# Kernel optimization log

Measured on AMD Instinct MI355X. Metric: run time of the kernel, lower is better.

The kernel has to match this reference:

```python
import jax, jax.numpy as jnp
import numpy as np

B, N, F_IN = 32, 1024, 64   # batch, num_nodes, diffusion_size[0]
K = 3                        # expansion_step
H = 2                        # num_heads
HID, RAW, OUT, CLS = 128, 128, 128, 2
D1, D2 = 128, 128            # diffusion_size[1], diffusion_size[2]
CAT = D1 + RAW               # concat dim fed to attention (h || h_prime) = 256


def setup_inputs() -> dict:
    key = jax.random.key(0)
    ks = jax.random.split(key, 40)
    g = lambda i, shape: jax.random.normal(ks[i], shape, dtype=jnp.float32) * 0.05
    inp = {
        'X': jax.random.normal(ks[0], (B, N, F_IN), dtype=jnp.float32),
        'A': jax.random.uniform(ks[1], (B, N, N), dtype=jnp.float32),
        # transition tensors / mixing weights (only the 2 layers used in forward)
        'T': g(2, (2, K, N, N)),
        'theta': jnp.full((2, K), 1.0 / K, dtype=jnp.float32),
        # raw feature projection
        'W_raw': g(3, (F_IN, RAW)), 'b_raw': jnp.zeros((RAW,), jnp.float32),
        # diffusion layer linears
        'Wd0': g(4, (F_IN, D1)), 'bd0': jnp.zeros((D1,), jnp.float32),
        'Wd1': g(5, (D1, D2)),   'bd1': jnp.zeros((D2,), jnp.float32),
        # final classifier
        'W_fin': g(6, (OUT, CLS)), 'b_fin': jnp.zeros((CLS,), jnp.float32),
    }
    # two CatMultiAttn blocks: q/k/v projections (CAT->HID), out proj (HID->OUT)
    i = 7
    for l in range(2):
        for nm in ('q', 'k', 'v'):
            inp[f'W{nm}{l}'] = g(i, (CAT, HID)); i += 1
            inp[f'b{nm}{l}'] = jnp.zeros((HID,), jnp.float32)
        inp[f'Wo{l}'] = g(i, (HID, OUT)); i += 1
        inp[f'bo{l}'] = jnp.zeros((OUT,), jnp.float32)
    return inp


def _diffusion(theta_l, T_l, h, A, W, b):
    # Q = sum_k theta_k * T_k  (generalized graph diffusion transition)
    Q = jnp.einsum('k,kij->ij', theta_l, T_l)          # [N,N]
    S = Q[None, :, :] * A                               # [B,N,N] mask by adjacency
    z = jnp.einsum('bij,bjf->bif', S, h)                # diffuse features
    return jax.nn.relu(z @ W + b)


def _cat_attn(h, hp, Wq, bq, Wk, bk, Wv, bv, Wo, bo):
    # concatenate diffused + embedding features, multi-head self-attn over nodes
    x = jnp.concatenate([h, hp], axis=-1)               # [B,N,CAT]
    b, n, _ = x.shape
    q = (x @ Wq + bq).reshape(b, n, H, HID // H)
    k = (x @ Wk + bk).reshape(b, n, H, HID // H)
    v = (x @ Wv + bv).reshape(b, n, H, HID // H)
    scale = jnp.asarray(1.0 / np.sqrt(HID // H), x.dtype)
    s = jnp.einsum('bnhd,bmhd->bhnm', q, k) * scale     # [B,H,N,N]
    p = jax.nn.softmax(s, axis=-1)
    ctx = jnp.einsum('bhnm,bmhd->bnhd', p, v).reshape(b, n, HID)
    return jax.nn.relu(ctx @ Wo + bo)


def reference(X, A, T, theta, W_raw, b_raw, Wd0, bd0, Wd1, bd1,
              W_fin, b_fin,
              Wq0, bq0, Wk0, bk0, Wv0, bv0, Wo0, bo0,
              Wq1, bq1, Wk1, bk1, Wv1, bv1, Wo1, bo1):
    theta_soft = jax.nn.softmax(theta, axis=-1)         # [2,K]
    h_prime = X @ W_raw + b_raw                          # [B,N,RAW]
    # layer 0
    h = _diffusion(theta_soft[0], T[0], X, A, Wd0, bd0)  # [B,N,D1]
    h_prime = _cat_attn(h, h_prime, Wq0, bq0, Wk0, bk0, Wv0, bv0, Wo0, bo0)
    # layer 1 (residual fusion)
    h = _diffusion(theta_soft[1], T[1], h, A, Wd1, bd1)  # [B,N,D2]
    h_prime = h_prime + _cat_attn(h, h_prime, Wq1, bq1, Wk1, bk1, Wv1, bv1, Wo1, bo1)
    return h_prime @ W_fin + b_fin                       # [B,N,CLS]
```

## Files before the change

### kernel.cpp

```cpp
#include <hip/hip_runtime.h>
#include <hip/hip_bf16.h>

typedef __hip_bfloat16 bf16;
typedef __attribute__((ext_vector_type(8))) short s8b;
typedef __attribute__((ext_vector_type(4))) short s4b;
typedef __attribute__((ext_vector_type(4))) float f4;

#define BB   32
#define NN   1024
#define FIN  64
#define HEADS 2
#define DH   64
#define HIDD 128
#define SZQ  ((size_t)BB * NN * HIDD)

__device__ __forceinline__ ushort f2bf(float x) {
    bf16 h = __float2bfloat16(x);
    return *(ushort*)&h;
}
__device__ __forceinline__ float bfbits2f(ushort h) {
    union { uint u; float f; } c; c.u = (uint)h << 16; return c.f;
}
__device__ __forceinline__ uint pk_bf16(float lo, float hi) {
    return (uint)f2bf(lo) | ((uint)f2bf(hi) << 16);
// ... 2 lines not shown
union U4 { short s[4]; s4b v; };
union UQ { ushort u[8]; s8b v; };

__global__ __launch_bounds__(256) void setup_kernel(
        const float* __restrict__ raw, const float* __restrict__ d0,
        const float* __restrict__ d1,
        const float* __restrict__ q0w, const float* __restrict__ k0w,
        const float* __restrict__ v0w, const float* __restrict__ o0w,
        const float* __restrict__ q1w, const float* __restrict__ k1w,
        const float* __restrict__ v1w, const float* __restrict__ o1w,
        ushort* __restrict__ Whi, ushort* __restrict__ Wlo,
        const float* __restrict__ T, const float* __restrict__ theta,
        ushort* __restrict__ Q0hi, ushort* __restrict__ Q0lo,
        ushort* __restrict__ Q1hi, ushort* __restrict__ Q1lo,
        const float* __restrict__ X,
        ushort* __restrict__ XT_hi, ushort* __restrict__ XT_lo) {
    __shared__ float tile[64][65];
    const int bid = blockIdx.x;
    const int t = threadIdx.x;
    if (bid < 1024) {
        int id = bid * 256 + t;
        const float* src; int K, off;
        if      (id <   8192) { src = raw; K =  64; off = 0; }
        else if (id <  16384) { src = d0;  K =  64; off = 8192; }
        else if (id <  32768) { src = d1;  K = 128; off = 16384; }
        else if (id <  65536) { src = q0w; K = 256; off = 32768; }
        else if (id <  98304) { src = k0w; K = 256; off = 65536; }
        else if (id < 131072) { src = v0w; K = 256; off = 98304; }
        else if (id < 147456) { src = o0w; K = 128; off = 131072; }
        else if (id < 180224) { src = q1w; K = 256; off = 147456; }
        else if (id < 212992) { src = k1w; K = 256; off = 180224; }
        else if (id < 245760) { src = v1w; K = 256; off = 212992; }
        else                  { src = o1w; K = 128; off = 245760; }
        int il = id - off;
        int k = il >> 7, c = il & 127;
        float w = src[il];
        ushort h = f2bf(w);
        Whi[off + c * K + k] = h;
        Wlo[off + c * K + k] = f2bf(w - bfbits2f(h));
    } else if (bid < 1536) {
        const int tb = bid - 1024;
        const int b  = tb >> 4;
        const int n0 = (tb & 15) * 64;
        {
            int nl = t >> 2, f0 = (t & 3) * 16;
            const float* xp = X + ((size_t)b * NN + n0 + nl) * 64 + f0;
#pragma unroll
            for (int i = 0; i < 16; i += 4)
                *(float4*)&tile[nl][f0 + i] = *(const float4*)(xp + i);
        }
        __syncthreads();
        {
            int f = t >> 2, n1 = (t & 3) * 16;
            U8 h0, h1, l0, l1;
#pragma unroll
            for (int i = 0; i < 16; i++) {
                float v = tile[n1 + i][f];
                ushort hh = f2bf(v);
                ushort ll = f2bf(v - bfbits2f(hh));
                if (i < 8) { h0.s[i] = (short)hh; l0.s[i] = (short)ll; }
                else       { h1.s[i - 8] = (short)hh; l1.s[i - 8] = (short)ll; }
            }
            size_t gb = ((size_t)b * 64 + f) * NN + n0 + n1;
            *(s8b*)&XT_hi[gb]     = h0.v;  *(s8b*)&XT_hi[gb + 8] = h1.v;
            *(s8b*)&XT_lo[gb]     = l0.v;  *(s8b*)&XT_lo[gb + 8] = l1.v;
        }
    } else {
        const int layer = (bid < 2048) ? 0 : 1;
        ushort* Qhi = layer ? Q1hi : Q0hi;
        ushort* Qlo = layer ? Q1lo : Q0lo;
        float t0 = theta[layer * 3 + 0];
        float t1 = theta[layer * 3 + 1];
        float t2 = theta[layer * 3 + 2];
        float m  = fmaxf(t0, fmaxf(t1, t2));
        float e0 = expf(t0 - m), e1 = expf(t1 - m), e2 = expf(t2 - m);
        float inv = 1.0f / (e0 + e1 + e2);
        e0 *= inv; e1 *= inv; e2 *= inv;
        size_t base = ((size_t)((bid - 1536) & 511) * 256 + t) * 8;
        const float* Tl = T + (size_t)layer * 3 * NN * NN;
        U8 hi, lo;
#pragma unroll
        for (int i = 0; i < 8; i++) {
            float q = e0 * Tl[base + i]
                    + e1 * Tl[base + i + (size_t)NN * NN]
                    + e2 * Tl[base + i + (size_t)2 * NN * NN];
            ushort hh = f2bf(q);
            hi.s[i] = (short)hh;
            lo.s[i] = (short)f2bf(q - bfbits2f(hh));
        }
        *(s8b*)&Qhi[base] = hi.v;
        *(s8b*)&Qlo[base] = lo.v;
    }
}

template<int F, bool WRITE_HT>
__global__ __launch_bounds__(512, 4) void diff_dense_kernel(
        const ushort* __restrict__ Qhi, const ushort* __restrict__ Qlo,
        const float* __restrict__ A,
        const ushort* __restrict__ hT_hi, const ushort* __restrict__ hT_lo,
        const ushort* __restrict__ WT_hi, const ushort* __restrict__ WT_lo,
        const float* __restrict__ bias,
        float* __restrict__ hout,
        ushort* __restrict__ hiT, ushort* __restrict__ loT) {
    constexpr int SS  = 72;
    constexpr int NT  = F / 16;
    constexpr int NCW = NT / 4;
    constexpr int SZ2 = F + 8;
    constexpr int P1 = 2 * 64 * SS + 2 * F * SS;
    constexpr int P2 = 2 * 64 * SZ2 + 2 * 128 * 40;
    __shared__ short smem[(P1 > P2) ? P1 : P2];
    short* Shi = smem;
    short* Slo = Shi + 64 * SS;
    short* Hhi = Slo + 64 * SS;
    short* Hlo = Hhi + (size_t)F * SS;
    short* Zhi = smem;
    short* Zlo = Zhi + 64 * SZ2;
    short* Wsh = Zlo + 64 * SZ2;
    short* Wsl = Wsh + 128 * 40;

    const int bidx = blockIdx.x;
    const int u  = bidx >> 3;
    const int b  = (bidx & 7) + 8 * (u >> 4);
    const int i0 = (u & 15) * 64;
    const int t  = threadIdx.x;
    const int w  = t >> 6, lane = t & 63;
    const int quad = lane >> 4, c = lane & 15;
    const int rh = w >> 2;
    const int ch = w & 3;

    const int srow = t >> 3, scol = (t & 7) * 8;
    const float*  Ap = A   + ((size_t)b * NN + i0 + srow) * NN + scol;
    const ushort* Qh = Qhi + (size_t)(i0 + srow) * NN + scol;
    const ushort* Ql = Qlo + (size_t)(i0 + srow) * NN + scol;
    constexpr int HTR = 512 / F;
    constexpr int HJ  = 64 / HTR;
    constexpr int HV  = HJ / 8;
    const int hrow = t / HTR, hcol = (t % HTR) * HJ;
    const ushort* Hh = hT_hi + ((size_t)b * F + hrow) * NN + hcol;
    const ushort* Hl = hT_lo + ((size_t)b * F + hrow) * NN + hcol;

    f4 acc[2][NCW];
#pragma unroll
    for (int st = 0; st < 2; st++)
#pragma unroll
        for (int i = 0; i < NCW; i++) acc[st][i] = (f4){0.f, 0.f, 0.f, 0.f};

    float4 a0 = *(const float4*)Ap, a1 = *(const float4*)(Ap + 4);
    s8b hhv[HV], hlv[HV];
#pragma unroll
    for (int vv = 0; vv < HV; vv++) {
        hhv[vv] = *(const s8b*)(Hh + 8 * vv);
        hlv[vv] = *(const s8b*)(Hl + 8 * vv);
    }

#pragma unroll 1
    for (int j0 = 0; j0 < NN; j0 += 64) {
        UQ qh, ql;
        qh.v = *(const s8b*)(Qh + j0);
        ql.v = *(const s8b*)(Ql + j0);
        __syncthreads();
        {
            float av[8] = {a0.x, a0.y, a0.z, a0.w, a1.x, a1.y, a1.z, a1.w};
            U8 hi, lo;
#pragma unroll
            for (int i = 0; i < 8; i++) {
                float q = bfbits2f(qh.u[i]) + bfbits2f(ql.u[i]);
                float s = q * av[i];
                ushort hb = f2bf(s);
                hi.s[i] = (short)hb;
                lo.s[i] = (short)f2bf(s - bfbits2f(hb));
            }
            *(s8b*)&Shi[srow * SS + scol] = hi.v;
            *(s8b*)&Slo[srow * SS + scol] = lo.v;
#pragma unroll
            for (int vv = 0; vv < HV; vv++) {
                *(s8b*)&Hhi[hrow * SS + hcol + 8 * vv] = hhv[vv];
                *(s8b*)&Hlo[hrow * SS + hcol + 8 * vv] = hlv[vv];
            }
        }
        if (j0 + 64 < NN) {
            a0 = *(const float4*)(Ap + j0 + 64);
            a1 = *(const float4*)(Ap + j0 + 68);
#pragma unroll
            for (int vv = 0; vv < HV; vv++) {
                hhv[vv] = *(const s8b*)(Hh + j0 + 64 + 8 * vv);
                hlv[vv] = *(const s8b*)(Hl + j0 + 64 + 8 * vv);
            }
        }
        __syncthreads();

#pragma unroll
        for (int ks = 0; ks < 2; ks++) {
            s8b ah0 = *(const s8b*)&Shi[(32 * rh + c) * SS + ks * 32 + quad * 8];
            s8b al0 = *(const s8b*)&Slo[(32 * rh + c) * SS + ks * 32 + quad * 8];
            s8b ah1 = *(const s8b*)&Shi[(32 * rh + 16 + c) * SS + ks * 32 + quad * 8];
            s8b al1 = *(const s8b*)&Slo[(32 * rh + 16 + c) * SS + ks * 32 + quad * 8];
#pragma unroll
            for (int ctn = 0; ctn < NCW; ctn++) {
                const int nt = ch * NCW + ctn;
                s8b bhi = *(const s8b*)&Hhi[(nt * 16 + c) * SS + ks * 32 + quad * 8];
                s8b blo = *(const s8b*)&Hlo[(nt * 16 + c) * SS + ks * 32 + quad * 8];
                acc[0][ctn] = __builtin_amdgcn_mfma_f32_16x16x32_bf16(ah0, bhi, acc[0][ctn], 0, 0, 0);
                acc[0][ctn] = __builtin_amdgcn_mfma_f32_16x16x32_bf16(al0, bhi, acc[0][ctn], 0, 0, 0);
                acc[0][ctn] = __builtin_amdgcn_mfma_f32_16x16x32_bf16(ah0, blo, acc[0][ctn], 0, 0, 0);
                acc[1][ctn] = __builtin_amdgcn_mfma_f32_16x16x32_bf16(ah1, bhi, acc[1][ctn], 0, 0, 0);
                acc[1][ctn] = __builtin_amdgcn_mfma_f32_16x16x32_bf16(al1, bhi, acc[1][ctn], 0, 0, 0);
                acc[1][ctn] = __builtin_amdgcn_mfma_f32_16x16x32_bf16(ah1, blo, acc[1][ctn], 0, 0, 0);
            }
        }
    }

    __syncthreads();
#pragma unroll
    for (int st = 0; st < 2; st++)
#pragma unroll
        for (int ctn = 0; ctn < NCW; ctn++)
#pragma unroll
            for (int r = 0; r < 4; r++) {
                const int row = 32 * rh + 16 * st + quad * 4 + r;
                const int col = (ch * NCW + ctn) * 16 + c;
                float v = acc[st][ctn][r];
                ushort hh = f2bf(v);
                Zhi[row * SZ2 + col] = (short)hh;
                Zlo[row * SZ2 + col] = (short)f2bf(v - bfbits2f(hh));
            }

    const int rh2 = w >> 2;
    const int ch2 = w & 3;
    f4 acc2[2][2];
#pragma unroll
    for (int st = 0; st < 2; st++)
#pragma unroll
        for (int i = 0; i < 2; i++) acc2[st][i] = (f4){0.f, 0.f, 0.f, 0.f};

    constexpr int NKT = F / 32;
    for (int kt = 0; kt < NKT; kt++) {
        __syncthreads();
        {
            int cc = t >> 2, kk = (t & 3) * 8;
            size_t gsrc = (size_t)cc * F + kt * 32 + kk;
            *(s8b*)&Wsh[cc * 40 + kk] = *(const s8b*)&WT_hi[gsrc];
            *(s8b*)&Wsl[cc * 40 + kk] = *(const s8b*)&WT_lo[gsrc];
        }
        __syncthreads();

        s8b ah0 = *(const s8b*)&Zhi[(32 * rh2 + c) * SZ2 + kt * 32 + quad * 8];
        s8b al0 = *(const s8b*)&Zlo[(32 * rh2 + c) * SZ2 + kt * 32 + quad * 8];
        s8b ah1 = *(const s8b*)&Zhi[(32 * rh2 + 16 + c) * SZ2 + kt * 32 + quad * 8];
        s8b al1 = *(const s8b*)&Zlo[(32 * rh2 + 16 + c) * SZ2 + kt * 32 + quad * 8];
#pragma unroll
        for (int ct = 0; ct < 2; ct++) {
            s8b bh = *(const s8b*)&Wsh[(ch2 * 32 + ct * 16 + c) * 40 + quad * 8];
            s8b bl = *(const s8b*)&Wsl[(ch2 * 32 + ct * 16 + c) * 40 + quad * 8];
            acc2[0][ct] = __builtin_amdgcn_mfma_f32_16x16x32_bf16(ah0, bh, acc2[0][ct], 0, 0, 0);
            acc2[0][ct] = __builtin_amdgcn_mfma_f32_16x16x32_bf16(al0, bh, acc2[0][ct], 0, 0, 0);
            acc2[0][ct] = __builtin_amdgcn_mfma_f32_16x16x32_bf16(ah0, bl, acc2[0][ct], 0, 0, 0);
            acc2[1][ct] = __builtin_amdgcn_mfma_f32_16x16x32_bf16(ah1, bh, acc2[1][ct], 0, 0, 0);
            acc2[1][ct] = __builtin_amdgcn_mfma_f32_16x16x32_bf16(al1, bh, acc2[1][ct], 0, 0, 0);
            acc2[1][ct] = __builtin_amdgcn_mfma_f32_16x16x32_bf16(ah1, bl, acc2[1][ct], 0, 0, 0);
        }
    }

#pragma unroll
    for (int st = 0; st < 2; st++) {
        const int rg0 = i0 + 32 * rh2 + 16 * st + quad * 4;
#pragma unroll
        for (int ct = 0; ct < 2; ct++) {
            const int col = ch2 * 32 + ct * 16 + c;
            float bv = bias[col];
            float vv[4];
#pragma unroll
            for (int r = 0; r < 4; r++) {
                float v = fmaxf(acc2[st][ct][r] + bv, 0.f);
                hout[((size_t)b * NN + rg0 + r) * 128 + col] = v;
                vv[r] = v;
            }
            if (WRITE_HT) {
                U4 ph, pl;
#pragma unroll
                for (int r = 0; r < 4; r++) {
                    ushort hh = f2bf(vv[r]);
                    ph.s[r] = (short)hh;
                    pl.s[r] = (short)f2bf(vv[r] - bfbits2f(hh));
                }
                size_t tb = ((size_t)b * 128 + col) * NN + rg0;
                *(s4b*)&hiT[tb] = ph.v;
                *(s4b*)&loT[tb] = pl.v;
            }
        }
    }
}

template<int K1, int K2, int CB, bool RELU, bool RESID, int OMODE>
__global__ __launch_bounds__(512) void dense_mfma_kernel(
        const float* __restrict__ in1, const float* __restrict__ in2,
        const ushort* __restrict__ WT_hi, const ushort* __restrict__ WT_lo,
        const float* __restrict__ bias, const float* __restrict__ biask,
        const float* __restrict__ biasv,
        float* __restrict__ out, ushort* __restrict__ outq,
        const float* __restrict__ Wfin, const float* __restrict__ bfin,
        float* __restrict__ fout) {
    constexpr int KD  = K1 + K2;
    constexpr int NKT = KD / 32;
    constexpr int NCH = CB / 32;
    __shared__ short Xhi[128][40], Xlo[128][40];
    __shared__ short Whi[CB][40], Wlo[CB][40];
    __shared__ float red[128][2];

    int bx, by;
    if (OMODE == 1) {
        const int xcd = blockIdx.x & 7, qq = blockIdx.x >> 3;
        by = qq & 1;
        bx = ((qq >> 1) << 3) | xcd;
    } else { bx = blockIdx.x; by = blockIdx.y; }
    const int r0 = bx * 128;
    const int c0 = by * CB;
    const int t  = threadIdx.x;
    const int w  = t >> 6, lane = t & 63;
    const int quad = lane >> 4, c = lane & 15;
    const int rh = w >> 1;
    const int ch = w & 1;

    f4 acc[2][NCH];
#pragma unroll
    for (int st = 0; st < 2; st++)
#pragma unroll
        for (int i = 0; i < NCH; i++) acc[st][i] = (f4){0.f, 0.f, 0.f, 0.f};

    for (int kt = 0; kt < NKT; kt++) {
        const int k0 = kt * 32;
        __syncthreads();
        {
            int row = t >> 2, kk = (t & 3) * 8;
            int g = r0 + row;
            const float* p;
            if (K2 > 0) {
                int k = k0 + kk;
                p = (k < K1) ? (in1 + (size_t)g * K1 + k)
                             : (in2 + (size_t)g * K2 + (k - K1));
            } else {
                p = in1 + (size_t)g * K1 + k0 + kk;
            }
            float4 a = *(const float4*)p, bq = *(const float4*)(p + 4);
            float sv[8] = {a.x, a.y, a.z, a.w, bq.x, bq.y, bq.z, bq.w};
            U8 hi, lo;
#pragma unroll
            for (int i = 0; i < 8; i++) {
                ushort hh = f2bf(sv[i]);
                hi.s[i] = (short)hh;
                lo.s[i] = (short)f2bf(sv[i] - bfbits2f(hh));
            }
            *(s8b*)&Xhi[row][kk] = hi.v;
            *(s8b*)&Xlo[row][kk] = lo.v;
        }
        {
            for (int id = t; id < CB * 4; id += 512) {
                int cc = id >> 2, kk = (id & 3) * 8;
                size_t gsrc = (size_t)(c0 + cc) * KD + k0 + kk;
                *(s8b*)&Whi[cc][kk] = *(const s8b*)&WT_hi[gsrc];
                *(s8b*)&Wlo[cc][kk] = *(const s8b*)&WT_lo[gsrc];
            }
        }
        __syncthreads();

        s8b ah0 = *(const s8b*)&Xhi[32 * rh + c][quad * 8];
        s8b al0 = *(const s8b*)&Xlo[32 * rh + c][quad * 8];
        s8b ah1 = *(const s8b*)&Xhi[32 * rh + 16 + c][quad * 8];
        s8b al1 = *(const s8b*)&Xlo[32 * rh + 16 + c][quad * 8];
#pragma unroll
        for (int ct = 0; ct < NCH; ct++) {
            s8b bh = *(const s8b*)&Whi[ch * (CB / 2) + ct * 16 + c][quad * 8];
            s8b bl = *(const s8b*)&Wlo[ch * (CB / 2) + ct * 16 + c][quad * 8];
            acc[0][ct] = __builtin_amdgcn_mfma_f32_16x16x32_bf16(ah0, bh, acc[0][ct], 0, 0, 0);
            acc[0][ct] = __builtin_amdgcn_mfma_f32_16x16x32_bf16(al0, bh, acc[0][ct], 0, 0, 0);
            acc[0][ct] = __builtin_amdgcn_mfma_f32_16x16x32_bf16(ah0, bl, acc[0][ct], 0, 0, 0);
            acc[1][ct] = __builtin_amdgcn_mfma_f32_16x16x32_bf16(ah1, bh, acc[1][ct], 0, 0, 0);
            acc[1][ct] = __builtin_amdgcn_mfma_f32_16x16x32_bf16(al1, bh, acc[1][ct], 0, 0, 0);
            acc[1][ct] = __builtin_amdgcn_mfma_f32_16x16x32_bf16(ah1, bl, acc[1][ct], 0, 0, 0);
        }
    }

    if (OMODE == 3) {
        float fc[2][2][4];
#pragma unroll
        for (int st = 0; st < 2; st++)
#pragma unroll
            for (int o = 0; o < 2; o++)
#pragma unroll
                for (int r = 0; r < 4; r++) fc[st][o][r] = 0.f;
#pragma unroll
        for (int ct = 0; ct < NCH; ct++) {
            const int col = c0 + ch * (CB / 2) + ct * 16 + c;
            float bv = bias[col];
            float w0 = Wfin[col * 2], w1 = Wfin[col * 2 + 1];
#pragma unroll
            for (int st = 0; st < 2; st++) {
                const int rg = r0 + 32 * rh + 16 * st + quad * 4;
#pragma unroll
                for (int r = 0; r < 4; r++) {
                    float v = acc[st][ct][r] + bv;
                    if (RELU) v = fmaxf(v, 0.f);
                    if (RESID) v += out[(size_t)(rg + r) * 128 + col];
                    fc[st][0][r] += v * w0;
                    fc[st][1][r] += v * w1;
                }
            }
        }
#pragma unroll
        for (int st = 0; st < 2; st++)
#pragma unroll
            for (int r = 0; r < 4; r++) {
                float a0 = fc[st][0][r], a1 = fc[st][1][r];
#pragma unroll
                for (int off = 1; off < 16; off <<= 1) {
                    a0 += __shfl_xor(a0, off, 16);
                    a1 += __shfl_xor(a1, off, 16);
                }
                fc[st][0][r] = a0; fc[st][1][r] = a1;
            }
        if (ch == 1 && c == 0) {
#pragma unroll
            for (int st = 0; st < 2; st++)
#pragma unroll
                for (int r = 0; r < 4; r++) {
                    int lr = 32 * rh + 16 * st + quad * 4 + r;
                    red[lr][0] = fc[st][0][r];
                    red[lr][1] = fc[st][1][r];
                }
        }
        __syncthreads();
        if (ch == 0 && c == 0) {
#pragma unroll
            for (int st = 0; st < 2; st++)
#pragma unroll
                for (int r = 0; r < 4; r++) {
                    int lr = 32 * rh + 16 * st + quad * 4 + r;
                    size_t row = (size_t)r0 + lr;
                    fout[row * 2]     = fc[st][0][r] + red[lr][0] + bfin[0];
                    fout[row * 2 + 1] = fc[st][1][r] + red[lr][1] + bfin[1];
                }
        }
        return;
    }
#pragma unroll
    for (int st = 0; st < 2; st++) {
        const int row_g0 = r0 + 32 * rh + 16 * st + quad * 4;
#pragma unroll
        for (int ct = 0; ct < NCH; ct++) {
            const int col = c0 + ch * (CB / 2) + ct * 16 + c;
            if (OMODE == 1) {
                int tensor = col >> 7, cc2 = col & 127;
                float bv = (tensor == 0 ? bias : tensor == 1 ? biask : biasv)[cc2];
                int head = cc2 >> 6, d = cc2 & 63;
                int b = row_g0 >> 10, n = row_g0 & 1023;
                if (tensor == 2) {
                    U4 pk;
#pragma unroll
                    for (int r = 0; r < 4; r++) pk.s[r] = (short)f2bf(acc[st][ct][r] + bv);
                    size_t addr = (((size_t)b * HEADS + head) * 64 + d) * NN + n;
                    *(s4b*)&outq[2 * SZQ + addr] = pk.v;
                } else {
                    ushort* dst = outq + (size_t)tensor * SZQ
                                + (((size_t)b * HEADS + head) * NN + n) * 64 + d;
#pragma unroll
                    for (int r = 0; r < 4; r++) dst[(size_t)r * 64] = f2bf(acc[st][ct][r] + bv);
                }
            } else {
                float bv = bias[col];
#pragma unroll
                for (int r = 0; r < 4; r++) {
                    float v = acc[st][ct][r] + bv;
                    if (RELU) v = fmaxf(v, 0.f);
                    size_t o = (size_t)(row_g0 + r) * 128 + col;
                    if (RESID) v += out[o];
                    out[o] = v;
                }
            }
        }
    }
}

__global__ __launch_bounds__(512) void attn_mfma_kernel(const ushort* __restrict__ q,
                                                        const ushort* __restrict__ k,
                                                        const ushort* __restrict__ vt,
                                                        float* __restrict__ ctx) {
    __shared__ short Ks[128][72];
    __shared__ short Vt[64][136];

    const int bidx = blockIdx.x;
    const int u  = bidx >> 3;
    const int bh = (bidx & 7) + 8 * (u >> 3);
    const int n0 = (u & 7) * 128;
    const int b  = bh >> 1, h = bh & 1;
    const int t  = threadIdx.x;
    const int w  = t >> 6;
    const int lane = t & 63;
    const int quad = lane >> 4, c = lane & 15;
    const size_t kvbase = (size_t)bh * NN * 64;
    const float scale = 0.125f;

    s8b qf0, qf1;
    {
        const ushort* qrow = q + kvbase + (size_t)(n0 + 16 * w + c) * 64;
        qf0 = *(const s8b*)(qrow + quad * 8);
        qf1 = *(const s8b*)(qrow + 32 + quad * 8);
    }

    f4 O[4];
#pragma unroll
    for (int i = 0; i < 4; i++) O[i] = (f4){0.f, 0.f, 0.f, 0.f};
    float l_i = 0.f;

    for (int kt0 = 0; kt0 < NN; kt0 += 128) {
        __syncthreads();
        {
            int key = t >> 2, d0 = (t & 3) * 16;
            const ushort* kr = k + kvbase + (size_t)(kt0 + key) * 64 + d0;
            *(s8b*)&Ks[key][d0]     = *(const s8b*)kr;
            *(s8b*)&Ks[key][d0 + 8] = *(const s8b*)(kr + 8);
            int d = t >> 3, chv = (t & 7) * 16;
            const ushort* vr = vt + kvbase + (size_t)d * NN + kt0 + chv;
            *(s8b*)&Vt[d][chv]     = *(const s8b*)vr;
            *(s8b*)&Vt[d][chv + 8] = *(const s8b*)(vr + 8);
        }
        __syncthreads();

        f4 sg[4][2];
#pragma unroll
        for (int g = 0; g < 4; g++) {
            const int kb = g * 32;
            sg[g][0] = (f4){0.f, 0.f, 0.f, 0.f};
            sg[g][1] = (f4){0.f, 0.f, 0.f, 0.f};
#pragma unroll
            for (int ch = 0; ch < 2; ch++) {
                s8b ka = *(const s8b*)&Ks[kb + c][ch * 32 + quad * 8];
                s8b kB = *(const s8b*)&Ks[kb + 16 + c][ch * 32 + quad * 8];
                s8b qf = ch ? qf1 : qf0;
                sg[g][0] = __builtin_amdgcn_mfma_f32_16x16x32_bf16(ka, qf, sg[g][0], 0, 0, 0);
                sg[g][1] = __builtin_amdgcn_mfma_f32_16x16x32_bf16(kB, qf, sg[g][1], 0, 0, 0);
            }
        }
        float pv[4][8];
        float ps = 0.f;
#pragma unroll
        for (int g = 0; g < 4; g++)
#pragma unroll
            for (int r = 0; r < 4; r++) {
                pv[g][r]     = __expf(sg[g][0][r] * scale);
                pv[g][4 + r] = __expf(sg[g][1][r] * scale);
                ps += pv[g][r] + pv[g][4 + r];
            }
        ps += __shfl_xor(ps, 16);
        ps += __shfl_xor(ps, 32);
        l_i += ps;

        int addr0 = ((((2 * quad) & 3) << 4) | c) << 2;
        int addr1 = ((((2 * quad + 1) & 3) << 4) | c) << 2;
        int tsel = quad >> 1;
#pragma unroll
        for (int g = 0; g < 4; g++) {
            const int kb = g * 32;
            uint Da01 = pk_bf16(pv[g][0], pv[g][1]), Da23 = pk_bf16(pv[g][2], pv[g][3]);
            uint Db01 = pk_bf16(pv[g][4], pv[g][5]), Db23 = pk_bf16(pv[g][6], pv[g][7]);
            int A01_0 = __builtin_amdgcn_ds_bpermute(addr0, (int)Da01);
            int A23_0 = __builtin_amdgcn_ds_bpermute(addr0, (int)Da23);
            int B01_0 = __builtin_amdgcn_ds_bpermute(addr0, (int)Db01);
            int B23_0 = __builtin_amdgcn_ds_bpermute(addr0, (int)Db23);
            int A01_1 = __builtin_amdgcn_ds_bpermute(addr1, (int)Da01);
            int A23_1 = __builtin_amdgcn_ds_bpermute(addr1, (int)Da23);
            int B01_1 = __builtin_amdgcn_ds_bpermute(addr1, (int)Db01);
            int B23_1 = __builtin_amdgcn_ds_bpermute(addr1, (int)Db23);
            union { int i[4]; s8b s; } pf;
            pf.i[0] = tsel ? B01_0 : A01_0;
            pf.i[1] = tsel ? B23_0 : A23_0;
            pf.i[2] = tsel ? B01_1 : A01_1;
            pf.i[3] = tsel ? B23_1 : A23_1;
#pragma unroll
            for (int dt = 0; dt < 4; dt++) {
                s8b vf = *(const s8b*)&Vt[16 * dt + c][kb + quad * 8];
                O[dt] = __builtin_amdgcn_mfma_f32_16x16x32_bf16(vf, pf.s, O[dt], 0, 0, 0);
            }
        }
    }

    float inv = 1.0f / l_i;
    float* crow = ctx + ((size_t)b * NN + n0 + 16 * w + c) * HIDD + h * DH;
#pragma unroll
    for (int dt = 0; dt < 4; dt++)
#pragma unroll
        for (int r = 0; r < 4; r++)
            crow[16 * dt + 4 * quad + r] = O[dt][r] * inv;
}

extern "C" void kernel_launch(void* const* d_in, const int* in_sizes, int n_in,
                              void* d_out, int out_size, void* d_ws, size_t ws_size,
                              hipStream_t stream) {
    (void)in_sizes; (void)n_in; (void)out_size; (void)ws_size;
    const float* X     = (const float*)d_in[0];
    const float* A     = (const float*)d_in[1];
    const float* T     = (const float*)d_in[2];
    const float* theta = (const float*)d_in[3];
    const float* W_raw = (const float*)d_in[4];
    const float* b_raw = (const float*)d_in[5];
    const float* Wd0   = (const float*)d_in[6];
    const float* bd0   = (const float*)d_in[7];
    const float* Wd1   = (const float*)d_in[8];
    const float* bd1   = (const float*)d_in[9];
    const float* W_fin = (const float*)d_in[10];
    const float* b_fin = (const float*)d_in[11];
    const float* Wq0 = (const float*)d_in[12]; const float* bq0 = (const float*)d_in[13];
    const float* Wk0 = (const float*)d_in[14]; const float* bk0 = (const float*)d_in[15];
    const float* Wv0 = (const float*)d_in[16]; const float* bv0 = (const float*)d_in[17];
    const float* Wo0 = (const float*)d_in[18]; const float* bo0 = (const float*)d_in[19];
    const float* Wq1 = (const float*)d_in[20]; const float* bq1 = (const float*)d_in[21];
    const float* Wk1 = (const float*)d_in[22]; const float* bk1 = (const float*)d_in[23];
    const float* Wv1 = (const float*)d_in[24]; const float* bv1 = (const float*)d_in[25];
    const float* Wo1 = (const float*)d_in[26]; const float* bo1 = (const float*)d_in[27];

    float* ws   = (float*)d_ws;
    const size_t SZ = (size_t)BB * NN * HIDD;
    ushort* Q0hi = (ushort*)ws;
    ushort* Q0lo = Q0hi + (size_t)NN * NN;
    float* hp   = ws + (size_t)NN * NN;
    float* h    = hp + SZ;
    float* z    = h + SZ;
    ushort* qb  = (ushort*)(z + SZ);
    ushort* kb  = qb + SZ;
    ushort* XT_hi = qb + 3 * SZ;
    ushort* XT_lo = XT_hi + SZ / 2;
    ushort* hT_hi = XT_lo + SZ / 2;
    ushort* hT_lo = hT_hi + SZ;
    ushort* WT_hi = hT_lo + SZ;
    ushort* WT_lo = WT_hi + 262144;
    ushort* Q1hi = WT_lo + 262144;
    ushort* Q1lo = Q1hi + (size_t)NN * NN;

    const int OFF_RAW = 0, OFF_D0 = 8192, OFF_D1 = 16384, OFF_QKV0 = 32768,
              OFF_O0 = 131072, OFF_QKV1 = 147456, OFF_O1 = 245760;

    const int attnGrid = BB * HEADS * (NN / 128);
    const int diffGrid = BB * (NN / 64);
    const dim3 dg1(256, 1);

    setup_kernel<<<2560, 256, 0, stream>>>(W_raw, Wd0, Wd1, Wq0, Wk0, Wv0, Wo0,
                                           Wq1, Wk1, Wv1, Wo1, WT_hi, WT_lo,
                                           T, theta, Q0hi, Q0lo, Q1hi, Q1lo,
                                           X, XT_hi, XT_lo);

    dense_mfma_kernel<64, 0, 128, false, false, 0><<<dg1, 512, 0, stream>>>(
        X, nullptr, WT_hi + OFF_RAW, WT_lo + OFF_RAW, b_raw, nullptr, nullptr,
        hp, nullptr, nullptr, nullptr, nullptr);
    diff_dense_kernel<64, true><<<diffGrid, 512, 0, stream>>>(
        Q0hi, Q0lo, A, XT_hi, XT_lo, WT_hi + OFF_D0, WT_lo + OFF_D0, bd0,
        h, hT_hi, hT_lo);
    dense_mfma_kernel<128, 128, 192, false, false, 1><<<512, 512, 0, stream>>>(
        h, hp, WT_hi + OFF_QKV0, WT_lo + OFF_QKV0, bq0, bk0, bv0,
        nullptr, qb, nullptr, nullptr, nullptr);
    attn_mfma_kernel<<<attnGrid, 512, 0, stream>>>(qb, kb, qb + 2 * SZ, z);
    dense_mfma_kernel<128, 0, 128, true, false, 0><<<dg1, 512, 0, stream>>>(
        z, nullptr, WT_hi + OFF_O0, WT_lo + OFF_O0, bo0, nullptr, nullptr,
        hp, nullptr, nullptr, nullptr, nullptr);

    diff_dense_kernel<128, false><<<diffGrid, 512, 0, stream>>>(
        Q1hi, Q1lo, A, hT_hi, hT_lo, WT_hi + OFF_D1, WT_lo + OFF_D1, bd1,
        h, nullptr, nullptr);
    dense_mfma_kernel<128, 128, 192, false, false, 1><<<512, 512, 0, stream>>>(
        h, hp, WT_hi + OFF_QKV1, WT_lo + OFF_QKV1, bq1, bk1, bv1,
        nullptr, qb, nullptr, nullptr, nullptr);
    attn_mfma_kernel<<<attnGrid, 512, 0, stream>>>(qb, kb, qb + 2 * SZ, z);
    dense_mfma_kernel<128, 0, 128, true, true, 3><<<dg1, 512, 0, stream>>>(
        z, nullptr, WT_hi + OFF_O1, WT_lo + OFF_O1, bo1, nullptr, nullptr,
        hp, nullptr, W_fin, b_fin, (float*)d_out);
}
```

Baseline: 484.2 us.

## Register-prefetch next global tiles across diffusion, dense and attention kernels

Adds software prefetching into registers: the next iteration's global loads (Q rows, W tiles, X activations, K/V tiles) are issued before the barrier and MFMA work of the current tile, then stored to LDS at the start of the next iteration. This is meant to hide global-memory latency behind compute in the diffusion, dense-projection and flash-attention loops. It costs extra live registers, which may lower occupancy.

```diff
diff --git a/kernel.cpp b/kernel.cpp
--- a/kernel.cpp
+++ b/kernel.cpp
@@ -178,12 +178,12 @@
         hhv[vv] = *(const s8b*)(Hh + 8 * vv);
         hlv[vv] = *(const s8b*)(Hl + 8 * vv);
     }
+    UQ qh, ql;
+    qh.v = *(const s8b*)Qh;
+    ql.v = *(const s8b*)Ql;
 
 #pragma unroll 1
     for (int j0 = 0; j0 < NN; j0 += 64) {
-        UQ qh, ql;
-        qh.v = *(const s8b*)(Qh + j0);
-        ql.v = *(const s8b*)(Ql + j0);
         __syncthreads();
         {
             float av[8] = {a0.x, a0.y, a0.z, a0.w, a1.x, a1.y, a1.z, a1.w};
@@ -212,6 +212,8 @@
                 hhv[vv] = *(const s8b*)(Hh + j0 + 64 + 8 * vv);
                 hlv[vv] = *(const s8b*)(Hl + j0 + 64 + 8 * vv);
             }
+            qh.v = *(const s8b*)(Qh + j0 + 64);
+            ql.v = *(const s8b*)(Ql + j0 + 64);
         }
         __syncthreads();
 
@@ -260,13 +262,17 @@
         for (int i = 0; i < 2; i++) acc2[st][i] = (f4){0.f, 0.f, 0.f, 0.f};
 
     constexpr int NKT = F / 32;
+    const int wcc = t >> 2, wkk = (t & 3) * 8;
+    s8b pwh = *(const s8b*)&WT_hi[(size_t)wcc * F + wkk];
+    s8b pwl = *(const s8b*)&WT_lo[(size_t)wcc * F + wkk];
     for (int kt = 0; kt < NKT; kt++) {
         __syncthreads();
-        {
-            int cc = t >> 2, kk = (t & 3) * 8;
-            size_t gsrc = (size_t)cc * F + kt * 32 + kk;
-            *(s8b*)&Wsh[cc * 40 + kk] = *(const s8b*)&WT_hi[gsrc];
-            *(s8b*)&Wsl[cc * 40 + kk] = *(const s8b*)&WT_lo[gsrc];
+        *(s8b*)&Wsh[wcc * 40 + wkk] = pwh;
+        *(s8b*)&Wsl[wcc * 40 + wkk] = pwl;
+        if (kt + 1 < NKT) {
+            size_t gsrc = (size_t)wcc * F + (kt + 1) * 32 + wkk;
+            pwh = *(const s8b*)&WT_hi[gsrc];
+            pwl = *(const s8b*)&WT_lo[gsrc];
         }
         __syncthreads();
 
@@ -329,6 +335,8 @@
     constexpr int KD  = K1 + K2;
     constexpr int NKT = KD / 32;
     constexpr int NCH = CB / 32;
+    constexpr int WCH = CB * 4;
+    constexpr int WPT = (WCH + 511) / 512;
     __shared__ short Xhi[128][40], Xlo[128][40];
     __shared__ short Whi[CB][40], Wlo[CB][40];
     __shared__ float red[128][2];
@@ -353,22 +361,41 @@
 #pragma unroll
         for (int i = 0; i < NCH; i++) acc[st][i] = (f4){0.f, 0.f, 0.f, 0.f};
 
+    const int xrow = t >> 2, xkk = (t & 3) * 8;
+    float4 pa, pbq;
+    s8b pwh[WPT], pwl[WPT];
+
+    auto loadX = [&](int k0) {
+        int g = r0 + xrow;
+        const float* p;
+        if (K2 > 0) {
+            int k = k0 + xkk;
+            p = (k < K1) ? (in1 + (size_t)g * K1 + k)
+                         : (in2 + (size_t)g * K2 + (k - K1));
+        } else {
+            p = in1 + (size_t)g * K1 + k0 + xkk;
+        }
+        pa = *(const float4*)p; pbq = *(const float4*)(p + 4);
+    };
+    auto loadW = [&](int k0) {
+#pragma unroll
+        for (int i = 0; i < WPT; i++) {
+            int id = t + i * 512;
+            if ((WCH % 512 == 0) || id < WCH) {
+                int cc = id >> 2, kk = (id & 3) * 8;
+                size_t gsrc = (size_t)(c0 + cc) * KD + k0 + kk;
+                pwh[i] = *(const s8b*)&WT_hi[gsrc];
+                pwl[i] = *(const s8b*)&WT_lo[gsrc];
+            }
+        }
+    };
+    loadX(0); loadW(0);
+
     for (int kt = 0; kt < NKT; kt++) {
         const int k0 = kt * 32;
         __syncthreads();
         {
-            int row = t >> 2, kk = (t & 3) * 8;
-            int g = r0 + row;
-            const float* p;
-            if (K2 > 0) {
-                int k = k0 + kk;
-                p = (k < K1) ? (in1 + (size_t)g * K1 + k)
-                             : (in2 + (size_t)g * K2 + (k - K1));
-            } else {
-                p = in1 + (size_t)g * K1 + k0 + kk;
-            }
-            float4 a = *(const float4*)p, bq = *(const float4*)(p + 4);
-            float sv[8] = {a.x, a.y, a.z, a.w, bq.x, bq.y, bq.z, bq.w};
+            float sv[8] = {pa.x, pa.y, pa.z, pa.w, pbq.x, pbq.y, pbq.z, pbq.w};
             U8 hi, lo;
 #pragma unroll
             for (int i = 0; i < 8; i++) {
@@ -376,17 +403,21 @@
                 hi.s[i] = (short)hh;
                 lo.s[i] = (short)f2bf(sv[i] - bfbits2f(hh));
             }
-            *(s8b*)&Xhi[row][kk] = hi.v;
-            *(s8b*)&Xlo[row][kk] = lo.v;
+            *(s8b*)&Xhi[xrow][xkk] = hi.v;
+            *(s8b*)&Xlo[xrow][xkk] = lo.v;
         }
         {
-            for (int id = t; id < CB * 4; id += 512) {
-                int cc = id >> 2, kk = (id & 3) * 8;
-                size_t gsrc = (size_t)(c0 + cc) * KD + k0 + kk;
-                *(s8b*)&Whi[cc][kk] = *(const s8b*)&WT_hi[gsrc];
-                *(s8b*)&Wlo[cc][kk] = *(const s8b*)&WT_lo[gsrc];
-            }
-        }
+#pragma unroll
+            for (int i = 0; i < WPT; i++) {
+                int id = t + i * 512;
+                if ((WCH % 512 == 0) || id < WCH) {
+                    int cc = id >> 2, kk = (id & 3) * 8;
+                    *(s8b*)&Whi[cc][kk] = pwh[i];
+                    *(s8b*)&Wlo[cc][kk] = pwl[i];
+                }
+            }
+        }
+        if (kt + 1 < NKT) { loadX(k0 + 32); loadW(k0 + 32); }
         __syncthreads();
 
         s8b ah0 = *(const s8b*)&Xhi[32 * rh + c][quad * 8];
@@ -537,18 +568,28 @@
     for (int i = 0; i < 4; i++) O[i] = (f4){0.f, 0.f, 0.f, 0.f};
     float l_i = 0.f;
 
+    const int skey = t >> 2, sd0 = (t & 3) * 16;
+    const int svd  = t >> 3, svc = (t & 7) * 16;
+    s8b pk0, pk1, pv0, pv1;
+    auto loadKV = [&](int kt0) {
+        const ushort* kr = k + kvbase + (size_t)(kt0 + skey) * 64 + sd0;
+        pk0 = *(const s8b*)kr;
+        pk1 = *(const s8b*)(kr + 8);
+        const ushort* vr = vt + kvbase + (size_t)svd * NN + kt0 + svc;
+        pv0 = *(const s8b*)vr;
+        pv1 = *(const s8b*)(vr + 8);
+    };
+    loadKV(0);
+
     for (int kt0 = 0; kt0 < NN; kt0 += 128) {
         __syncthreads();
         {
-            int key = t >> 2, d0 = (t & 3) * 16;
-            const ushort* kr = k + kvbase + (size_t)(kt0 + key) * 64 + d0;
-            *(s8b*)&Ks[key][d0]     = *(const s8b*)kr;
-            *(s8b*)&Ks[key][d0 + 8] = *(const s8b*)(kr + 8);
-            int d = t >> 3, chv = (t & 7) * 16;
-            const ushort* vr = vt + kvbase + (size_t)d * NN + kt0 + chv;
-            *(s8b*)&Vt[d][chv]     = *(const s8b*)vr;
-            *(s8b*)&Vt[d][chv + 8] = *(const s8b*)(vr + 8);
-        }
+            *(s8b*)&Ks[skey][sd0]     = pk0;
+            *(s8b*)&Ks[skey][sd0 + 8] = pk1;
+            *(s8b*)&Vt[svd][svc]      = pv0;
+            *(s8b*)&Vt[svd][svc + 8]  = pv1;
+        }
+        if (kt0 + 128 < NN) loadKV(kt0 + 128);
         __syncthreads();
 
         f4 sg[4][2];
```

Result: no change. 490.7 us (+1.3%).

## Fuse attention with output projection and final classifier into one kernel

Applied to the files above, without the earlier changes.

Replaces the separate attention kernel and the following dense output-projection kernels with one kernel per (batch, 128-row) tile. It loops over both heads, stages the normalized context in shared memory as hi/lo bf16, and applies Wo (and for the last layer the residual plus classifier) in place. This removes the fp32 ctx round-trip through global memory and two kernel launches. In exchange the grid halves, each block does both heads serially, and the larger shared memory footprint reduces occupancy.

```diff
diff --git a/kernel.cpp b/kernel.cpp
--- a/kernel.cpp
+++ b/kernel.cpp
@@ -323,15 +323,12 @@
         const ushort* __restrict__ WT_hi, const ushort* __restrict__ WT_lo,
         const float* __restrict__ bias, const float* __restrict__ biask,
         const float* __restrict__ biasv,
-        float* __restrict__ out, ushort* __restrict__ outq,
-        const float* __restrict__ Wfin, const float* __restrict__ bfin,
-        float* __restrict__ fout) {
+        float* __restrict__ out, ushort* __restrict__ outq) {
     constexpr int KD  = K1 + K2;
     constexpr int NKT = KD / 32;
     constexpr int NCH = CB / 32;
     __shared__ short Xhi[128][40], Xlo[128][40];
     __shared__ short Whi[CB][40], Wlo[CB][40];
-    __shared__ float red[128][2];
 
     int bx, by;
     if (OMODE == 1) {
@@ -406,68 +403,6 @@
         }
     }
 
-    if (OMODE == 3) {
-        float fc[2][2][4];
-#pragma unroll
-        for (int st = 0; st < 2; st++)
-#pragma unroll
-            for (int o = 0; o < 2; o++)
-#pragma unroll
-                for (int r = 0; r < 4; r++) fc[st][o][r] = 0.f;
-#pragma unroll
-        for (int ct = 0; ct < NCH; ct++) {
-            const int col = c0 + ch * (CB / 2) + ct * 16 + c;
-            float bv = bias[col];
-            float w0 = Wfin[col * 2], w1 = Wfin[col * 2 + 1];
-#pragma unroll
-            for (int st = 0; st < 2; st++) {
-                const int rg = r0 + 32 * rh + 16 * st + quad * 4;
-#pragma unroll
-                for (int r = 0; r < 4; r++) {
-                    float v = acc[st][ct][r] + bv;
-                    if (RELU) v = fmaxf(v, 0.f);
-                    if (RESID) v += out[(size_t)(rg + r) * 128 + col];
-                    fc[st][0][r] += v * w0;
-                    fc[st][1][r] += v * w1;
-                }
-            }
-        }
-#pragma unroll
-        for (int st = 0; st < 2; st++)
-#pragma unroll
-            for (int r = 0; r < 4; r++) {
-                float a0 = fc[st][0][r], a1 = fc[st][1][r];
-#pragma unroll
-                for (int off = 1; off < 16; off <<= 1) {
-                    a0 += __shfl_xor(a0, off, 16);
-                    a1 += __shfl_xor(a1, off, 16);
-                }
-                fc[st][0][r] = a0; fc[st][1][r] = a1;
-            }
-        if (ch == 1 && c == 0) {
-#pragma unroll
-            for (int st = 0; st < 2; st++)
-#pragma unroll
-                for (int r = 0; r < 4; r++) {
-                    int lr = 32 * rh + 16 * st + quad * 4 + r;
-                    red[lr][0] = fc[st][0][r];
-                    red[lr][1] = fc[st][1][r];
-                }
-        }
-        __syncthreads();
-        if (ch == 0 && c == 0) {
-#pragma unroll
-            for (int st = 0; st < 2; st++)
-#pragma unroll
-                for (int r = 0; r < 4; r++) {
-                    int lr = 32 * rh + 16 * st + quad * 4 + r;
-                    size_t row = (size_t)r0 + lr;
-                    fout[row * 2]     = fc[st][0][r] + red[lr][0] + bfin[0];
-                    fout[row * 2 + 1] = fc[st][1][r] + red[lr][1] + bfin[1];
-                }
-        }
-        return;
-    }
 #pragma unroll
     for (int st = 0; st < 2; st++) {
         const int row_g0 = r0 + 32 * rh + 16 * st + quad * 4;
@@ -506,116 +441,262 @@
     }
 }
 
-__global__ __launch_bounds__(512) void attn_mfma_kernel(const ushort* __restrict__ q,
-                                                        const ushort* __restrict__ k,
-                                                        const ushort* __restrict__ vt,
-                                                        float* __restrict__ ctx) {
-    __shared__ short Ks[128][72];
-    __shared__ short Vt[64][136];
+template<bool FINAL>
+__global__ __launch_bounds__(512) void attn_oproj_kernel(
+        const ushort* __restrict__ q, const ushort* __restrict__ k,
+        const ushort* __restrict__ vt,
+        const ushort* __restrict__ WoT_hi, const ushort* __restrict__ WoT_lo,
+        const float* __restrict__ bo,
+        float* __restrict__ hp,
+        const float* __restrict__ Wfin, const float* __restrict__ bfin,
+        float* __restrict__ fout) {
+    constexpr int ZS = 136;
+    constexpr int PB = 2 * 128 * ZS + 2 * 128 * 40 + 512;
+    __shared__ short smem[PB];
+    short* Ks  = smem;
+    short* Vt  = smem + 128 * 72;
+    short* Zhi = smem;
+    short* Zlo = Zhi + 128 * ZS;
+    short* Wsh = Zlo + 128 * ZS;
+    short* Wsl = Wsh + 128 * 40;
+    float* red = (float*)(Wsl + 128 * 40);
 
     const int bidx = blockIdx.x;
     const int u  = bidx >> 3;
-    const int bh = (bidx & 7) + 8 * (u >> 3);
+    const int b  = (bidx & 7) + 8 * (u >> 3);
     const int n0 = (u & 7) * 128;
-    const int b  = bh >> 1, h = bh & 1;
     const int t  = threadIdx.x;
     const int w  = t >> 6;
     const int lane = t & 63;
     const int quad = lane >> 4, c = lane & 15;
-    const size_t kvbase = (size_t)bh * NN * 64;
     const float scale = 0.125f;
 
-    s8b qf0, qf1;
+    const int skey = t >> 2, sd0 = (t & 3) * 16;
+    const int svd  = t >> 3, svc = (t & 7) * 16;
+
+    f4 Oh[2][4];
+    float li[2];
+
+#pragma unroll
+    for (int h = 0; h < 2; h++) {
+        const size_t kvbase = ((size_t)(b * HEADS + h)) * NN * 64;
+        s8b qf0, qf1;
+        {
+            const ushort* qrow = q + kvbase + (size_t)(n0 + 16 * w + c) * 64;
+            qf0 = *(const s8b*)(qrow + quad * 8);
+            qf1 = *(const s8b*)(qrow + 32 + quad * 8);
+        }
+        f4 O[4];
+#pragma unroll
+        for (int i = 0; i < 4; i++) O[i] = (f4){0.f, 0.f, 0.f, 0.f};
+        float l_i = 0.f;
+
+        for (int kt0 = 0; kt0 < NN; kt0 += 128) {
+            __syncthreads();
+            {
+                const ushort* kr = k + kvbase + (size_t)(kt0 + skey) * 64 + sd0;
+                *(s8b*)&Ks[skey * 72 + sd0]     = *(const s8b*)kr;
+                *(s8b*)&Ks[skey * 72 + sd0 + 8] = *(const s8b*)(kr + 8);
+                const ushort* vr = vt + kvbase + (size_t)svd * NN + kt0 + svc;
+                *(s8b*)&Vt[svd * 136 + svc]     = *(const s8b*)vr;
+                *(s8b*)&Vt[svd * 136 + svc + 8] = *(const s8b*)(vr + 8);
+            }
+            __syncthreads();
+
+            f4 sg[4][2];
+#pragma unroll
+            for (int g = 0; g < 4; g++) {
+                const int kb = g * 32;
+                sg[g][0] = (f4){0.f, 0.f, 0.f, 0.f};
+                sg[g][1] = (f4){0.f, 0.f, 0.f, 0.f};
+#pragma unroll
+                for (int ck = 0; ck < 2; ck++) {
+                    s8b ka = *(const s8b*)&Ks[(kb + c) * 72 + ck * 32 + quad * 8];
+                    s8b kB = *(const s8b*)&Ks[(kb + 16 + c) * 72 + ck * 32 + quad * 8];
+                    s8b qf = ck ? qf1 : qf0;
+                    sg[g][0] = __builtin_amdgcn_mfma_f32_16x16x32_bf16(ka, qf, sg[g][0], 0, 0, 0);
+                    sg[g][1] = __builtin_amdgcn_mfma_f32_16x16x32_bf16(kB, qf, sg[g][1], 0, 0, 0);
+                }
+            }
+            float pv[4][8];
+            float ps = 0.f;
+#pragma unroll
+            for (int g = 0; g < 4; g++)
+#pragma unroll
+                for (int r = 0; r < 4; r++) {
+                    pv[g][r]     = __expf(sg[g][0][r] * scale);
+                    pv[g][4 + r] = __expf(sg[g][1][r] * scale);
+                    ps += pv[g][r] + pv[g][4 + r];
+                }
+            ps += __shfl_xor(ps, 16);
+            ps += __shfl_xor(ps, 32);
+            l_i += ps;
+
+            int addr0 = ((((2 * quad) & 3) << 4) | c) << 2;
+            int addr1 = ((((2 * quad + 1) & 3) << 4) | c) << 2;
+            int tsel = quad >> 1;
+#pragma unroll
+            for (int g = 0; g < 4; g++) {
+                const int kb = g * 32;
+                uint Da01 = pk_bf16(pv[g][0], pv[g][1]), Da23 = pk_bf16(pv[g][2], pv[g][3]);
+                uint Db01 = pk_bf16(pv[g][4], pv[g][5]), Db23 = pk_bf16(pv[g][6], pv[g][7]);
+                int A01_0 = __builtin_amdgcn_ds_bpermute(addr0, (int)Da01);
+                int A23_0 = __builtin_amdgcn_ds_bpermute(addr0, (int)Da23);
+                int B01_0 = __builtin_amdgcn_ds_bpermute(addr0, (int)Db01);
+                int B23_0 = __builtin_amdgcn_ds_bpermute(addr0, (int)Db23);
+                int A01_1 = __builtin_amdgcn_ds_bpermute(addr1, (int)Da01);
+                int A23_1 = __builtin_amdgcn_ds_bpermute(addr1, (int)Da23);
+                int B01_1 = __builtin_amdgcn_ds_bpermute(addr1, (int)Db01);
+                int B23_1 = __builtin_amdgcn_ds_bpermute(addr1, (int)Db23);
+                union { int i[4]; s8b s; } pf;
+                pf.i[0] = tsel ? B01_0 : A01_0;
+                pf.i[1] = tsel ? B23_0 : A23_0;
+                pf.i[2] = tsel ? B01_1 : A01_1;
+                pf.i[3] = tsel ? B23_1 : A23_1;
+#pragma unroll
+                for (int dt = 0; dt < 4; dt++) {
+                    s8b vf = *(const s8b*)&Vt[(16 * dt + c) * 136 + kb + quad * 8];
+                    O[dt] = __builtin_amdgcn_mfma_f32_16x16x32_bf16(vf, pf.s, O[dt], 0, 0, 0);
+                }
+            }
+        }
+        li[h] = 1.0f / l_i;
+#pragma unroll
+        for (int dt = 0; dt < 4; dt++) Oh[h][dt] = O[dt];
+    }
+
+    __syncthreads();
     {
-        const ushort* qrow = q + kvbase + (size_t)(n0 + 16 * w + c) * 64;
-        qf0 = *(const s8b*)(qrow + quad * 8);
-        qf1 = *(const s8b*)(qrow + 32 + quad * 8);
-    }
-
-    f4 O[4];
-#pragma unroll
-    for (int i = 0; i < 4; i++) O[i] = (f4){0.f, 0.f, 0.f, 0.f};
-    float l_i = 0.f;
-
-    for (int kt0 = 0; kt0 < NN; kt0 += 128) {
+        const int zrow = 16 * w + c;
+#pragma unroll
+        for (int h = 0; h < 2; h++) {
+            float inv = li[h];
+#pragma unroll
+            for (int dt = 0; dt < 4; dt++) {
+                U4 ph, pl;
+#pragma unroll
+                for (int r = 0; r < 4; r++) {
+                    float v = Oh[h][dt][r] * inv;
+                    ushort hh = f2bf(v);
+                    ph.s[r] = (short)hh;
+                    pl.s[r] = (short)f2bf(v - bfbits2f(hh));
+                }
+                int col = h * 64 + 16 * dt + 4 * quad;
+                *(s4b*)&Zhi[zrow * ZS + col] = ph.v;
+                *(s4b*)&Zlo[zrow * ZS + col] = pl.v;
+            }
+        }
+    }
+
+    const int rh = w >> 1;
+    const int ch = w & 1;
+    f4 acc[2][4];
+#pragma unroll
+    for (int st = 0; st < 2; st++)
+#pragma unroll
+        for (int i = 0; i < 4; i++) acc[st][i] = (f4){0.f, 0.f, 0.f, 0.f};
+
+    for (int kt = 0; kt < 4; kt++) {
         __syncthreads();
         {
-            int key = t >> 2, d0 = (t & 3) * 16;
-            const ushort* kr = k + kvbase + (size_t)(kt0 + key) * 64 + d0;
-            *(s8b*)&Ks[key][d0]     = *(const s8b*)kr;
-            *(s8b*)&Ks[key][d0 + 8] = *(const s8b*)(kr + 8);
-            int d = t >> 3, chv = (t & 7) * 16;
-            const ushort* vr = vt + kvbase + (size_t)d * NN + kt0 + chv;
-            *(s8b*)&Vt[d][chv]     = *(const s8b*)vr;
-            *(s8b*)&Vt[d][chv + 8] = *(const s8b*)(vr + 8);
-        }
-        __syncthreads();
-
-        f4 sg[4][2];
-#pragma unroll
-        for (int g = 0; g < 4; g++) {
-            const int kb = g * 32;
-            sg[g][0] = (f4){0.f, 0.f, 0.f, 0.f};
-            sg[g][1] = (f4){0.f, 0.f, 0.f, 0.f};
-#pragma unroll
-            for (int ch = 0; ch < 2; ch++) {
-                s8b ka = *(const s8b*)&Ks[kb + c][ch * 32 + quad * 8];
-                s8b kB = *(const s8b*)&Ks[kb + 16 + c][ch * 32 + quad * 8];
-                s8b qf = ch ? qf1 : qf0;
-                sg[g][0] = __builtin_amdgcn_mfma_f32_16x16x32_bf16(ka, qf, sg[g][0], 0, 0, 0);
-                sg[g][1] = __builtin_amdgcn_mfma_f32_16x16x32_bf16(kB, qf, sg[g][1], 0, 0, 0);
-            }
-        }
-        float pv[4][8];
-        float ps = 0.f;
-#pragma unroll
-        for (int g = 0; g < 4; g++)
+            int cc = t >> 2, kk = (t & 3) * 8;
+            size_t gsrc = (size_t)cc * 128 + kt * 32 + kk;
+            *(s8b*)&Wsh[cc * 40 + kk] = *(const s8b*)&WoT_hi[gsrc];
+            *(s8b*)&Wsl[cc * 40 + kk] = *(const s8b*)&WoT_lo[gsrc];
+        }
+        __syncthreads();
+
+        s8b ah0 = *(const s8b*)&Zhi[(32 * rh + c) * ZS + kt * 32 + quad * 8];
+        s8b al0 = *(const s8b*)&Zlo[(32 * rh + c) * ZS + kt * 32 + quad * 8];
+        s8b ah1 = *(const s8b*)&Zhi[(32 * rh + 16 + c) * ZS + kt * 32 + quad * 8];
+        s8b al1 = *(const s8b*)&Zlo[(32 * rh + 16 + c) * ZS + kt * 32 + quad * 8];
+#pragma unroll
+        for (int ct = 0; ct < 4; ct++) {
+            s8b bh = *(const s8b*)&Wsh[(ch * 64 + ct * 16 + c) * 40 + quad * 8];
+            s8b bl = *(const s8b*)&Wsl[(ch * 64 + ct * 16 + c) * 40 + quad * 8];
+            acc[0][ct] = __builtin_amdgcn_mfma_f32_16x16x32_bf16(ah0, bh, acc[0][ct], 0, 0, 0);
+            acc[0][ct] = __builtin_amdgcn_mfma_f32_16x16x32_bf16(al0, bh, acc[0][ct], 0, 0, 0);
+            acc[0][ct] = __builtin_amdgcn_mfma_f32_16x16x32_bf16(ah0, bl, acc[0][ct], 0, 0, 0);
+            acc[1][ct] = __builtin_amdgcn_mfma_f32_16x16x32_bf16(ah1, bh, acc[1][ct], 0, 0, 0);
+            acc[1][ct] = __builtin_amdgcn_mfma_f32_16x16x32_bf16(al1, bh, acc[1][ct], 0, 0, 0);
+            acc[1][ct] = __builtin_amdgcn_mfma_f32_16x16x32_bf16(ah1, bl, acc[1][ct], 0, 0, 0);
+        }
+    }
+
+    if (FINAL) {
+        float fc[2][2][4];
+#pragma unroll
+        for (int st = 0; st < 2; st++)
+#pragma unroll
+            for (int o = 0; o < 2; o++)
+#pragma unroll
+                for (int r = 0; r < 4; r++) fc[st][o][r] = 0.f;
+#pragma unroll
+        for (int ct = 0; ct < 4; ct++) {
+            const int col = ch * 64 + ct * 16 + c;
+            float bv = bo[col];
+            float w0 = Wfin[col * 2], w1 = Wfin[col * 2 + 1];
+#pragma unroll
+            for (int st = 0; st < 2; st++) {
+                const size_t rg = (size_t)b * NN + n0 + 32 * rh + 16 * st + quad * 4;
+#pragma unroll
+                for (int r = 0; r < 4; r++) {
+                    float v = fmaxf(acc[st][ct][r] + bv, 0.f);
+                    v += hp[(rg + r) * 128 + col];
+                    fc[st][0][r] += v * w0;
+                    fc[st][1][r] += v * w1;
+                }
+            }
+        }
+#pragma unroll
+        for (int st = 0; st < 2; st++)
 #pragma unroll
             for (int r = 0; r < 4; r++) {
-                pv[g][r]     = __expf(sg[g][0][r] * scale);
-                pv[g][4 + r] = __expf(sg[g][1][r] * scale);
-                ps += pv[g][r] + pv[g][4 + r];
-            }
-        ps += __shfl_xor(ps, 16);
-        ps += __shfl_xor(ps, 32);
-        l_i += ps;
-
-        int addr0 = ((((2 * quad) & 3) << 4) | c) << 2;
-        int addr1 = ((((2 * quad + 1) & 3) << 4) | c) << 2;
-        int tsel = quad >> 1;
-#pragma unroll
-        for (int g = 0; g < 4; g++) {
-            const int kb = g * 32;
-            uint Da01 = pk_bf16(pv[g][0], pv[g][1]), Da23 = pk_bf16(pv[g][2], pv[g][3]);
-            uint Db01 = pk_bf16(pv[g][4], pv[g][5]), Db23 = pk_bf16(pv[g][6], pv[g][7]);
-            int A01_0 = __builtin_amdgcn_ds_bpermute(addr0, (int)Da01);
-            int A23_0 = __builtin_amdgcn_ds_bpermute(addr0, (int)Da23);
-            int B01_0 = __builtin_amdgcn_ds_bpermute(addr0, (int)Db01);
-            int B23_0 = __builtin_amdgcn_ds_bpermute(addr0, (int)Db23);
-            int A01_1 = __builtin_amdgcn_ds_bpermute(addr1, (int)Da01);
-            int A23_1 = __builtin_amdgcn_ds_bpermute(addr1, (int)Da23);
-            int B01_1 = __builtin_amdgcn_ds_bpermute(addr1, (int)Db01);
-            int B23_1 = __builtin_amdgcn_ds_bpermute(addr1, (int)Db23);
-            union { int i[4]; s8b s; } pf;
-            pf.i[0] = tsel ? B01_0 : A01_0;
-            pf.i[1] = tsel ? B23_0 : A23_0;
-            pf.i[2] = tsel ? B01_1 : A01_1;
-            pf.i[3] = tsel ? B23_1 : A23_1;
-#pragma unroll
-            for (int dt = 0; dt < 4; dt++) {
-                s8b vf = *(const s8b*)&Vt[16 * dt + c][kb + quad * 8];
-                O[dt] = __builtin_amdgcn_mfma_f32_16x16x32_bf16(vf, pf.s, O[dt], 0, 0, 0);
-            }
-        }
-    }
-
-    float inv = 1.0f / l_i;
-    float* crow = ctx + ((size_t)b * NN + n0 + 16 * w + c) * HIDD + h * DH;
-#pragma unroll
-    for (int dt = 0; dt < 4; dt++)
-#pragma unroll
-        for (int r = 0; r < 4; r++)
-            crow[16 * dt + 4 * quad + r] = O[dt][r] * inv;
+                float a0 = fc[st][0][r], a1 = fc[st][1][r];
+#pragma unroll
+                for (int off = 1; off < 16; off <<= 1) {
+                    a0 += __shfl_xor(a0, off, 16);
+                    a1 += __shfl_xor(a1, off, 16);
+                }
+                fc[st][0][r] = a0; fc[st][1][r] = a1;
+            }
+        if (ch == 1 && c == 0) {
+#pragma unroll
+            for (int st = 0; st < 2; st++)
+#pragma unroll
+                for (int r = 0; r < 4; r++) {
+                    int lr = 32 * rh + 16 * st + quad * 4 + r;
+                    red[lr * 2]     = fc[st][0][r];
+                    red[lr * 2 + 1] = fc[st][1][r];
+                }
+        }
+        __syncthreads();
+        if (ch == 0 && c == 0) {
+#pragma unroll
+            for (int st = 0; st < 2; st++)
+#pragma unroll
+                for (int r = 0; r < 4; r++) {
+                    int lr = 32 * rh + 16 * st + quad * 4 + r;
+                    size_t row = (size_t)b * NN + n0 + lr;
+                    fout[row * 2]     = fc[st][0][r] + red[lr * 2]     + bfin[0];
+                    fout[row * 2 + 1] = fc[st][1][r] + red[lr * 2 + 1] + bfin[1];
+                }
+        }
+        return;
+    }
+
+#pragma unroll
+    for (int st = 0; st < 2; st++) {
+        const size_t rg = (size_t)b * NN + n0 + 32 * rh + 16 * st + quad * 4;
+#pragma unroll
+        for (int ct = 0; ct < 4; ct++) {
+            const int col = ch * 64 + ct * 16 + c;
+            float bv = bo[col];
+#pragma unroll
+            for (int r = 0; r < 4; r++)
+                hp[(rg + r) * 128 + col] = fmaxf(acc[st][ct][r] + bv, 0.f);
+        }
+    }
 }
 
 extern "C" void kernel_launch(void* const* d_in, const int* in_sizes, int n_in,
@@ -664,7 +745,7 @@
     const int OFF_RAW = 0, OFF_D0 = 8192, OFF_D1 = 16384, OFF_QKV0 = 32768,
               OFF_O0 = 131072, OFF_QKV1 = 147456, OFF_O1 = 245760;
 
-    const int attnGrid = BB * HEADS * (NN / 128);
+    const int attnGrid = BB * (NN / 128);
     const int diffGrid = BB * (NN / 64);
     const dim3 dg1(256, 1);
 
@@ -675,26 +756,24 @@
 
     dense_mfma_kernel<64, 0, 128, false, false, 0><<<dg1, 512, 0, stream>>>(
         X, nullptr, WT_hi + OFF_RAW, WT_lo + OFF_RAW, b_raw, nullptr, nullptr,
-        hp, nullptr, nullptr, nullptr, nullptr);
+        hp, nullptr);
     diff_dense_kernel<64, true><<<diffGrid, 512, 0, stream>>>(
         Q0hi, Q0lo, A, XT_hi, XT_lo, WT_hi + OFF_D0, WT_lo + OFF_D0, bd0,
         h, hT_hi, hT_lo);
     dense_mfma_kernel<128, 128, 192, false, false, 1><<<512, 512, 0, stream>>>(
         h, hp, WT_hi + OFF_QKV0, WT_lo + OFF_QKV0, bq0, bk0, bv0,
-        nullptr, qb, nullptr, nullptr, nullptr);
-    attn_mfma_kernel<<<attnGrid, 512, 0, stream>>>(qb, kb, qb + 2 * SZ, z);
-    dense_mfma_kernel<128, 0, 128, true, false, 0><<<dg1, 512, 0, stream>>>(
-        z, nullptr, WT_hi + OFF_O0, WT_lo + OFF_O0, bo0, nullptr, nullptr,
-        hp, nullptr, nullptr, nullptr, nullptr);
+        nullptr, qb);
+    attn_oproj_kernel<false><<<attnGrid, 512, 0, stream>>>(
+        qb, kb, qb + 2 * SZ, WT_hi + OFF_O0, WT_lo + OFF_O0, bo0,
+        hp, nullptr, nullptr, nullptr);
 
     diff_dense_kernel<128, false><<<diffGrid, 512, 0, stream>>>(
         Q1hi, Q1lo, A, hT_hi, hT_lo, WT_hi + OFF_D1, WT_lo + OFF_D1, bd1,
         h, nullptr, nullptr);
     dense_mfma_kernel<128, 128, 192, false, false, 1><<<512, 512, 0, stream>>>(
         h, hp, WT_hi + OFF_QKV1, WT_lo + OFF_QKV1, bq1, bk1, bv1,
-        nullptr, qb, nullptr, nullptr, nullptr);
-    attn_mfma_kernel<<<attnGrid, 512, 0, stream>>>(qb, kb, qb + 2 * SZ, z);
-    dense_mfma_kernel<128, 0, 128, true, true, 3><<<dg1, 512, 0, stream>>>(
-        z, nullptr, WT_hi + OFF_O1, WT_lo + OFF_O1, bo1, nullptr, nullptr,
-        hp, nullptr, W_fin, b_fin, (float*)d_out);
+        nullptr, qb);
+    attn_oproj_kernel<true><<<attnGrid, 512, 0, stream>>>(
+        qb, kb, qb + 2 * SZ, WT_hi + OFF_O1, WT_lo + OFF_O1, bo1,
+        hp, W_fin, b_fin, (float*)d_out);
 }
```

After: 487.1 us. No clear change (+0.6%).
